# Performance work log

Measured on AMD Instinct MI355X. Metric: run time of the kernel, lower is better.

The kernel has to match this reference:

```python
import jax, jax.numpy as jnp
import numpy as np

# ----- config (matches init_kwargs) -----
DATA_SIZE = 128
WIDTH = 512
DEPTH = 3          # hidden layers in eqx.nn.MLP
NUM_BLOCKS = 2
BATCH = 512
NSTEPS = 10        # (t1 - t0) / dt0 = 1.0 / 0.1
T1 = 1.0
DT = -0.1          # integrate t1 -> t0

# Tsit5 Butcher tableau (5th-order solution weights; b7 = 0 so stage 7 is skipped)
TS_C = [0.0, 0.161, 0.327, 0.9, 0.9800255409045097, 1.0]
TS_A = [
    [],
    [0.161],
    [-0.008480655492356989, 0.335480655492357],
    [2.8971530571054935, -6.359448489975075, 4.3622954328695815],
    [5.325864828439257, -11.748883564062828, 7.4955393428898365, -0.09249506636175525],
    [5.86145544294642, -12.92096931784711, 8.159367898576159, -0.071584973281401, -0.028269050394068383],
]
TS_B = [0.09646076681806523, 0.01, 0.4798896504144996, 1.379008574103742, -3.290069515436081, 2.324710524099774]


def setup_inputs() -> dict:
    key = jax.random.key(0)
    ks = jax.random.split(key, 10)
    d, w, nb = DATA_SIZE, WIDTH, NUM_BLOCKS
    in0 = d + 1  # autonomous=False: t is concatenated to y

    def init(k, shape, fan_in):
        return jax.random.normal(k, shape, dtype=jnp.float32) / np.sqrt(fan_in).astype(np.float32)

    return {
        "y": jax.random.normal(ks[0], (BATCH, d), dtype=jnp.float32),
        "Ws0": init(ks[1], (nb, in0, w), in0), "bs0": init(ks[2], (nb, w), w),
        "Ws1": init(ks[3], (nb, w, w), w),     "bs1": init(ks[4], (nb, w), w),
        "Ws2": init(ks[5], (nb, w, w), w),     "bs2": init(ks[6], (nb, w), w),
        "Ws3": init(ks[7], (nb, w, d), w),     "bs3": init(ks[8], (nb, d), d),
    }


def _mlp(inp, layers):
    # inp: [in_size] vector (per-sample), relu hidden activations, linear output
    h = inp
    for W, b in layers[:-1]:
        h = jax.nn.relu(h @ W + b)
    W, b = layers[-1]
    return h @ W + b


def _field_and_trace(t, y, layers):
    # y: [B, d]. Exact log-det trace via vmapped vjp over identity (exact_logp_wrapper).
    eye = jnp.eye(DATA_SIZE, dtype=y.dtype)

    def single(yy):
        fn = lambda z: _mlp(jnp.concatenate([jnp.full((1,), t, yy.dtype), z]), layers)
        f, vjp_fn = jax.vjp(fn, yy)
        (dfdy,) = jax.vmap(vjp_fn)(eye)  # [d, d] Jacobian
        return f, jnp.trace(dfdy)

    return jax.vmap(single)(y)


def _solve_block(y, lp, layers):
    # Fixed-step Tsit5 on augmented state (y, logp), t1 -> t0, 10 steps.
    def step(carry, n):
        y, lp = carry
        t = jnp.float32(T1) + jnp.float32(DT) * n.astype(jnp.float32)
        ky, klp = [], []
        for i in range(6):
            ti = t + jnp.float32(TS_C[i] * DT)
            yi = y
            for j in range(i):
                yi = yi + jnp.float32(DT * TS_A[i][j]) * ky[j]
            fy, flp = _field_and_trace(ti, yi, layers)
            ky.append(fy)
            klp.append(flp)
        for i in range(6):
            y = y + jnp.float32(DT * TS_B[i]) * ky[i]
            lp = lp + jnp.float32(DT * TS_B[i]) * klp[i]
        return (y, lp), None

    (y, lp), _ = jax.lax.scan(step, (y, lp), jnp.arange(NSTEPS))
    return y, lp


def reference(y, Ws0, bs0, Ws1, bs1, Ws2, bs2, Ws3, bs3):
    lp = jnp.zeros((y.shape[0],), dtype=y.dtype)  # delta log-likelihood
    for b in range(NUM_BLOCKS):
        layers = [(Ws0[b], bs0[b]), (Ws1[b], bs1[b]), (Ws2[b], bs2[b]), (Ws3[b], bs3[b])]
        y, lp = _solve_block(y, lp, layers)
    # normal_log_likelihood (faithful to source: log(2*pi) NOT scaled by d)
    log2pi = np.float32(np.log(2.0 * np.pi))
    return lp + (-0.5) * (log2pi + jnp.sum(y * y, axis=-1))
```

## Files before the change

### kernel.cpp

```cpp
#include <hip/hip_runtime.h>


using short8 = __attribute__((ext_vector_type(8))) short;
using u16x8  = __attribute__((ext_vector_type(8))) unsigned short;
using f32x4v = __attribute__((ext_vector_type(4))) float;
using i32x4  = __attribute__((ext_vector_type(4))) int;
using u32x4  = __attribute__((ext_vector_type(4))) unsigned;

__device__ __forceinline__ unsigned short f2bf(float f) {
  union { float f; unsigned u; } v; v.f = f;
  unsigned r = v.u + 0x7fffu + ((v.u >> 16) & 1u);
  return (unsigned short)(r >> 16);
}
__device__ __forceinline__ float bf2f(unsigned short h) {
  union { unsigned u; float f; } v; v.u = ((unsigned)h) << 16; return v.f;
}
__device__ __forceinline__ signed char q8(float v, float inv) {
  float r = rintf(v * inv);
  r = fminf(fmaxf(r, -127.f), 127.f);
  return (signed char)(int)r;
}

typedef const __attribute__((address_space(1))) void gas_t;
typedef __attribute__((address_space(3))) void las_t;
__device__ __forceinline__ void gl_lds16(const void* g, void* l) {
  __builtin_amdgcn_global_load_lds((gas_t*)g, (las_t*)l, 16, 0, 0);
}

struct Coef5 { float v[5]; };
struct Coef6 { float v[6]; };

#define INV_S0 254.0f
#define INV_S1 508.0f
#define SCALE_J 7.7500155e-06f
#define SCALE_G 3.8750077e-06f

__global__ __launch_bounds__(256) void init_state(const float* __restrict__ y_in,
                                                  float* __restrict__ y,
                                                  float* __restrict__ lp) {
  int i = blockIdx.x * 256 + threadIdx.x;
  if (i < 512 * 128) y[i] = y_in[i];
  if (i < 512) lp[i] = 0.f;
}

__global__ __launch_bounds__(256) void cast_weights(
    const float* __restrict__ W0, const float* __restrict__ W1,
    const float* __restrict__ W2, const float* __restrict__ W3,
    signed char* __restrict__ w0q,
    unsigned short* __restrict__ w0tH, unsigned short* __restrict__ w0tL,
    unsigned short* __restrict__ w1tH, unsigned short* __restrict__ w1tL,
    signed char* __restrict__ w1q,
    unsigned short* __restrict__ w2tH, unsigned short* __restrict__ w2tL,
    unsigned short* __restrict__ w3tH, unsigned short* __restrict__ w3tL,
    signed char* __restrict__ w3q, signed char* __restrict__ w2q) {
  int i = blockIdx.x * 256 + threadIdx.x;
  if (i < 65536) {
    int j = i >> 9, a = i & 511;
    w0q[i] = q8(W0[(1 + j) * 512 + a], INV_S0);
    return;
  }
  i -= 65536;
  if (i >= 2 * 65536 + 2 * 262144) {
    int q = i - (2 * 65536 + 2 * 262144);
    if (q < 262144) w2q[q] = q8(W2[q], INV_S1);
    return;
  }
  float v;
  unsigned short* dh;
  unsigned short* dl;
  signed char* qd = nullptr;
  int di;
  if (i < 65536) {
    int n = i >> 7, k = i & 127;
    v = W0[(1 + k) * 512 + n]; dh = w0tH; dl = w0tL; di = i;
  } else if (i < 65536 + 262144) {
    int q = i - 65536; int n = q >> 9, k = q & 511;
    v = W1[k * 512 + n]; dh = w1tH; dl = w1tL; di = q; qd = w1q;
  } else if (i < 65536 + 2 * 262144) {
    int q = i - 65536 - 262144; int c = q >> 9, b = q & 511;
    v = W2[b * 512 + c]; dh = w2tH; dl = w2tL; di = q;
  } else {
    int q = i - 65536 - 2 * 262144; int j = q >> 9, c = q & 511;
    v = W3[c * 128 + j]; dh = w3tH; dl = w3tL; di = q; qd = w3q;
  }
  unsigned short hi = f2bf(v);
  dh[di] = hi;
  dl[di] = f2bf(v - bf2f(hi));
  if (qd) qd[di] = q8(v, INV_S1);
}

__global__ __launch_bounds__(256, 2) void fwd_l0(
    const float* __restrict__ yb, const float* __restrict__ kyb, Coef5 ca, int nc,
    const unsigned short* __restrict__ WtH, const unsigned short* __restrict__ WtL,
    const float* __restrict__ bias, const float* __restrict__ wrow0, float tval,
    unsigned short* __restrict__ Hhi, unsigned short* __restrict__ Hlo) {
  __shared__ unsigned short AsH[4096], AsL[4096], BsH[4096], BsL[4096];
  const int t = threadIdx.x, l = t & 63;
  const int wv = t >> 6, wm = wv >> 1, wn = wv & 1;
  const int lr = l & 15, lg = l >> 4, lr7 = lr & 7;
  const int m0 = blockIdx.y * 32, n0 = blockIdx.x * 32;

#pragma unroll
  for (int r = 0; r < 2; ++r) {
    int g = r * 256 + t;
    int row = g >> 4;
    int gc = (g & 15) ^ (row & 7);
    size_t bo = (size_t)(n0 + row) * 128 + gc * 8;
    int db = (r * 256 + (t & 192)) * 16;
    gl_lds16(WtH + bo, (char*)BsH + db);
    gl_lds16(WtL + bo, (char*)BsL + db);
  }
  {
    int row = t >> 3, seg = t & 7;
    int gidx = (m0 + row) * 128 + seg * 16;
    float x[16];
#pragma unroll
    for (int q = 0; q < 4; ++q) *(float4*)&x[q * 4] = *(const float4*)&yb[gidx + q * 4];
    for (int j2 = 0; j2 < nc; ++j2) {
      float c = ca.v[j2];
#pragma unroll
      for (int q = 0; q < 4; ++q) {
        float4 u = *(const float4*)&kyb[j2 * 65536 + gidx + q * 4];
        x[q * 4 + 0] = fmaf(c, u.x, x[q * 4 + 0]);
        x[q * 4 + 1] = fmaf(c, u.y, x[q * 4 + 1]);
        x[q * 4 + 2] = fmaf(c, u.z, x[q * 4 + 2]);
        x[q * 4 + 3] = fmaf(c, u.w, x[q * 4 + 3]);
      }
    }
    u16x8 h8[2], l8[2];
#pragma unroll
    for (int e = 0; e < 16; ++e) {
      unsigned short hh = f2bf(x[e]);
      h8[e >> 3][e & 7] = hh;
      l8[e >> 3][e & 7] = f2bf(x[e] - bf2f(hh));
    }
#pragma unroll
    for (int h = 0; h < 2; ++h) {
      int gx = (seg * 2 + h) ^ (row & 7);
      *(u16x8*)((char*)AsH + row * 256 + gx * 16) = h8[h];
      *(u16x8*)((char*)AsL + row * 256 + gx * 16) = l8[h];
    }
  }
  __syncthreads();

  f32x4v acc = {0.f, 0.f, 0.f, 0.f};
#pragma unroll
  for (int ks = 0; ks < 4; ++ks) {
    int sl = ((ks * 4 + lg) ^ lr7) << 4;
    int ab = (wm * 16 + lr) * 256 + sl;
    int bb = (wn * 16 + lr) * 256 + sl;
    short8 ah = *(const short8*)((const char*)AsH + ab);
    short8 al = *(const short8*)((const char*)AsL + ab);
    short8 bh = *(const short8*)((const char*)BsH + bb);
    short8 bl = *(const short8*)((const char*)BsL + bb);
    acc = __builtin_amdgcn_mfma_f32_16x16x32_bf16(ah, bh, acc, 0, 0, 0);
    acc = __builtin_amdgcn_mfma_f32_16x16x32_bf16(ah, bl, acc, 0, 0, 0);
    acc = __builtin_amdgcn_mfma_f32_16x16x32_bf16(al, bh, acc, 0, 0, 0);
  }

  int n = n0 + wn * 16 + lr;
  float be = fmaf(tval, wrow0[n], bias[n]);
#pragma unroll
  for (int r = 0; r < 4; ++r) {
    int m = m0 + wm * 16 + lg * 4 + r;
    float v = fmaxf(acc[r] + be, 0.f);
    unsigned short h = f2bf(v);
    Hhi[m * 512 + n] = h;
    Hlo[m * 512 + n] = f2bf(v - bf2f(h));
  }
}

template <bool RELU>
__global__ __launch_bounds__(256, 2) void fwd_mfma(
    const unsigned short* __restrict__ Ahi, const unsigned short* __restrict__ Alo,
    const unsigned short* __restrict__ WtH, const unsigned short* __restrict__ WtL,
    const float* __restrict__ bias,
    float* __restrict__ Cf, unsigned short* __restrict__ Hhi,
    unsigned short* __restrict__ Hlo, int N, int K) {
  __shared__ unsigned short AsH[2][4096], AsL[2][4096], BsH[2][4096], BsL[2][4096];
  const int t = threadIdx.x, l = t & 63, w = t >> 6;
  const int wm = w >> 1, wn = w & 1, lr = l & 15, lg = l >> 4;
  const int m0 = blockIdx.y * 32, n0 = blockIdx.x * 32;
  const int lr7 = lr & 7;

  auto stage = [&](int cur, int k0) {
#pragma unroll
    for (int r = 0; r < 2; ++r) {
      int g = r * 256 + t;
      int row = g >> 4, gc = g & 15;
      size_t co = (size_t)k0 + ((gc ^ (row & 7)) << 3);
      size_t ao = (size_t)(m0 + row) * K + co;
      size_t bo = (size_t)(n0 + row) * K + co;
      int db = (r * 256 + (t & 192)) * 16;
      gl_lds16(Ahi + ao, (char*)AsH[cur] + db);
      gl_lds16(Alo + ao, (char*)AsL[cur] + db);
      gl_lds16(WtH + bo, (char*)BsH[cur] + db);
      gl_lds16(WtL + bo, (char*)BsL[cur] + db);
    }
  };

  f32x4v acc = {0.f, 0.f, 0.f, 0.f};
  stage(0, 0);
  __syncthreads();
  int cur = 0;
  for (int k0 = 0; k0 < K; k0 += 128) {
    if (k0 + 128 < K) stage(cur ^ 1, k0 + 128);
#pragma unroll
    for (int ks = 0; ks < 4; ++ks) {
      int sl = ((ks * 4 + lg) ^ lr7) << 4;
      int ab = (wm * 16 + lr) * 256 + sl;
      int bb = (wn * 16 + lr) * 256 + sl;
      short8 ah = *(const short8*)((const char*)AsH[cur] + ab);
      short8 al = *(const short8*)((const char*)AsL[cur] + ab);
      short8 bh = *(const short8*)((const char*)BsH[cur] + bb);
      short8 bl = *(const short8*)((const char*)BsL[cur] + bb);
      acc = __builtin_amdgcn_mfma_f32_16x16x32_bf16(ah, bh, acc, 0, 0, 0);
      acc = __builtin_amdgcn_mfma_f32_16x16x32_bf16(ah, bl, acc, 0, 0, 0);
      acc = __builtin_amdgcn_mfma_f32_16x16x32_bf16(al, bh, acc, 0, 0, 0);
    }
    __syncthreads();
    cur ^= 1;
  }

  int n = n0 + wn * 16 + lr;
  float be = bias[n];
#pragma unroll
  for (int r = 0; r < 4; ++r) {
    int m = m0 + wm * 16 + lg * 4 + r;
    float v = acc[r] + be;
    if (RELU) {
      v = fmaxf(v, 0.f);
      unsigned short h = f2bf(v);
      Hhi[m * N + n] = h;
      Hlo[m * N + n] = f2bf(v - bf2f(h));
    } else {
      Cf[m * N + n] = v;
    }
  }
}

__global__ __launch_bounds__(256, 2) void jac_fused(
    const signed char* __restrict__ w1q, const signed char* __restrict__ w0q,
    const signed char* __restrict__ w2q, const signed char* __restrict__ w3q,
    const unsigned short* __restrict__ d0m, const unsigned short* __restrict__ d1m,
    const unsigned short* __restrict__ d2m, float* __restrict__ klp) {
  __shared__ signed char As[2][8192];
  __shared__ signed char Bs[2][8192];
  __shared__ unsigned char Ms8[3 * 2 * 512];
  __shared__ float red[8];
  const int cb = blockIdx.x, s0 = blockIdx.y * 2;
  const int t = threadIdx.x, l = t & 63, w = t >> 6;
  const int wm = w >> 1, wn = w & 1, lr = l & 15, lg = l >> 4;

  if (w < 3) {
    const unsigned short* src = (w == 0) ? d0m : (w == 1) ? d1m : d2m;
    gl_lds16(src + (size_t)s0 * 512 + l * 8, (void*)&As[0][w * 2048]);
    gl_lds16(src + (size_t)(s0 + 1) * 512 + l * 8, (void*)&As[0][w * 2048 + 1024]);
  }
  __syncthreads();
  {
    const unsigned* Mraw = (const unsigned*)&As[0][0];
    unsigned* Mout = (unsigned*)&Ms8[0];
#pragma unroll
    for (int q = 0; q < 3; ++q) {
      int i = q * 256 + t;
      unsigned lo = Mraw[2 * i], hi = Mraw[2 * i + 1];
      unsigned m = 0;
      if (lo & 0xFFFFu) m |= 0x000000FFu;
      if (lo >> 16)     m |= 0x0000FF00u;
      if (hi & 0xFFFFu) m |= 0x00FF0000u;
      if (hi >> 16)     m |= 0xFF000000u;
      Mout[i] = m;
    }
  }
  __syncthreads();

  auto stage = [&](int buf, const signed char* Aq, const signed char* Bq, int k0) {
#pragma unroll
    for (int i = 0; i < 4; ++i) {
      int u = i * 4 + w;
      if (u < 8) {
        int row = u * 16 + (l >> 2);
        gl_lds16(Aq + (size_t)(cb * 128 + row) * 512 + k0 + (l & 3) * 16,
                 (void*)&As[buf][u * 1024]);
      } else {
        int v2 = u - 8;
        int row = v2 * 16 + (l >> 2);
        gl_lds16(Bq + (size_t)row * 512 + k0 + (l & 3) * 16,
                 (void*)&Bs[buf][v2 * 1024]);
      }
    }
  };

  i32x4 a0[4][4], a1[4][4];
  auto phase = [&](const signed char* Aq, const signed char* Bq, int mbase) {
#pragma unroll
    for (int mt = 0; mt < 4; ++mt)
#pragma unroll
      for (int nt = 0; nt < 4; ++nt) {
        a0[mt][nt] = i32x4{0, 0, 0, 0};
        a1[mt][nt] = i32x4{0, 0, 0, 0};
      }
    stage(0, Aq, Bq, 0);
    __syncthreads();
    int cur = 0;
    for (int k0 = 0; k0 < 512; k0 += 64) {
      if (k0 + 64 < 512) stage(cur ^ 1, Aq, Bq, k0 + 64);
      i32x4 af[4];
#pragma unroll
      for (int mt = 0; mt < 4; ++mt)
        af[mt] = *(const i32x4*)&As[cur][(wm * 64 + mt * 16 + lr) * 64 + lg * 16];
      u32x4 mk0 = *(const u32x4*)&Ms8[mbase + k0 + lg * 16];
      u32x4 mk1 = *(const u32x4*)&Ms8[mbase + 512 + k0 + lg * 16];
#pragma unroll
      for (int nt = 0; nt < 4; ++nt) {
        u32x4 bv = *(const u32x4*)&Bs[cur][(wn * 64 + nt * 16 + lr) * 64 + lg * 16];
        i32x4 b0 = (i32x4)(bv & mk0);
        i32x4 b1 = (i32x4)(bv & mk1);
#pragma unroll
        for (int mt = 0; mt < 4; ++mt) {
          a0[mt][nt] = __builtin_amdgcn_mfma_i32_16x16x64_i8(af[mt], b0,
                                                             a0[mt][nt], 0, 0, 0);
          a1[mt][nt] = __builtin_amdgcn_mfma_i32_16x16x64_i8(af[mt], b1,
                                                             a1[mt][nt], 0, 0, 0);
        }
      }
      __syncthreads();
      cur ^= 1;
    }
  };

  phase(w2q, w3q, 2 * 1024);
  unsigned pg0[4][4][2], pg1[4][4][2];
#pragma unroll
  for (int mt = 0; mt < 4; ++mt)
#pragma unroll
    for (int nt = 0; nt < 4; ++nt) {
      float g00 = (float)a0[mt][nt][0] * SCALE_G, g01 = (float)a0[mt][nt][1] * SCALE_G;
      float g02 = (float)a0[mt][nt][2] * SCALE_G, g03 = (float)a0[mt][nt][3] * SCALE_G;
      float g10 = (float)a1[mt][nt][0] * SCALE_G, g11 = (float)a1[mt][nt][1] * SCALE_G;
      float g12 = (float)a1[mt][nt][2] * SCALE_G, g13 = (float)a1[mt][nt][3] * SCALE_G;
      asm("v_cvt_pk_bf16_f32 %0, %1, %2" : "=v"(pg0[mt][nt][0]) : "v"(g00), "v"(g01));
      asm("v_cvt_pk_bf16_f32 %0, %1, %2" : "=v"(pg0[mt][nt][1]) : "v"(g02), "v"(g03));
      asm("v_cvt_pk_bf16_f32 %0, %1, %2" : "=v"(pg1[mt][nt][0]) : "v"(g10), "v"(g11));
      asm("v_cvt_pk_bf16_f32 %0, %1, %2" : "=v"(pg1[mt][nt][1]) : "v"(g12), "v"(g13));
    }

  phase(w1q, w0q, 0);

  float p0 = 0.f, p1 = 0.f;
  const unsigned char* D1b = &Ms8[1 * 1024];
#pragma unroll
  for (int mt = 0; mt < 4; ++mt) {
    int bl = wm * 64 + mt * 16 + lg * 4;
    int blg = cb * 128 + bl;
    uchar4 m40 = *(const uchar4*)&D1b[blg];
    uchar4 m41 = *(const uchar4*)&D1b[512 + blg];
    unsigned char mm0[4] = {m40.x, m40.y, m40.z, m40.w};
    unsigned char mm1[4] = {m41.x, m41.y, m41.z, m41.w};
#pragma unroll
    for (int r = 0; r < 4; ++r) {
#pragma unroll
      for (int nt = 0; nt < 4; ++nt) {
        unsigned pw0 = pg0[mt][nt][r >> 1];
        unsigned pw1 = pg1[mt][nt][r >> 1];
        unsigned short g0 = (r & 1) ? (unsigned short)(pw0 >> 16)
                                    : (unsigned short)(pw0 & 0xFFFFu);
        unsigned short g1 = (r & 1) ? (unsigned short)(pw1 >> 16)
                                    : (unsigned short)(pw1 & 0xFFFFu);
        if (mm0[r]) p0 = fmaf((float)a0[mt][nt][r], bf2f(g0), p0);
        if (mm1[r]) p1 = fmaf((float)a1[mt][nt][r], bf2f(g1), p1);
      }
    }
  }
  p0 *= SCALE_J;
  p1 *= SCALE_J;
#pragma unroll
  for (int off = 1; off < 64; off <<= 1) {
    p0 += __shfl_xor(p0, off);
    p1 += __shfl_xor(p1, off);
  }
  if (l == 0) { red[w * 2] = p0; red[w * 2 + 1] = p1; }
  __syncthreads();
  if (t < 2) {
    klp[cb * 512 + s0 + t] = red[t] + red[2 + t] + red[4 + t] + red[6 + t];
  }
}

__global__ __launch_bounds__(256) void step_update(float* __restrict__ y,
                                                   float* __restrict__ lp,
                                                   const float* __restrict__ ky,
                                                   const float* __restrict__ klp_part,
                                                   Coef6 db) {
  int i = blockIdx.x * 256 + threadIdx.x;
  if (i < 65536) {
    float a = y[i];
#pragma unroll
    for (int j = 0; j < 6; ++j) a += db.v[j] * ky[j * 65536 + i];
    y[i] = a;
  }
  if (i < 512) {
    float l = lp[i];
#pragma unroll
    for (int j = 0; j < 6; ++j) {
      const float* kp = klp_part + j * 2048;
      float tr = kp[i] + kp[512 + i] + kp[1024 + i] + kp[1536 + i];
      l += db.v[j] * tr;
    }
    lp[i] = l;
  }
}

__global__ __launch_bounds__(64) void finalize(const float* __restrict__ y,
                                               const float* __restrict__ lp,
                                               float* __restrict__ out) {
  int s = blockIdx.x, l = threadIdx.x;
  float v0 = y[s * 128 + l], v1 = y[s * 128 + 64 + l];
  float sum = v0 * v0 + v1 * v1;
#pragma unroll
  for (int off = 32; off; off >>= 1) sum += __shfl_down(sum, off);
  if (l == 0) out[s] = lp[s] + (-0.5f) * (1.8378770664093453f + sum);
}

extern "C" void kernel_launch(void* const* d_in, const int* in_sizes, int n_in,
                              void* d_out, int out_size, void* d_ws, size_t ws_size,
                              hipStream_t stream) {
  const float* y_in = (const float*)d_in[0];
  const float* Ws0 = (const float*)d_in[1];
  const float* bs0 = (const float*)d_in[2];
  const float* Ws1 = (const float*)d_in[3];
  const float* bs1 = (const float*)d_in[4];
  const float* Ws2 = (const float*)d_in[5];
  const float* bs2 = (const float*)d_in[6];
  const float* Ws3 = (const float*)d_in[7];
  const float* bs3 = (const float*)d_in[8];
  float* out = (float*)d_out;

  char* ws = (char*)d_ws;
  size_t off = 0;
  auto alloc = [&](size_t bytes) {
    void* p = ws + off;
    off = (off + bytes + 255) & ~(size_t)255;
    return p;
  };
  float* y  = (float*)alloc(65536 * 4);
  float* lp = (float*)alloc(512 * 4);
  unsigned short* h0hi = (unsigned short*)alloc(262144 * 2);
  unsigned short* h0lo = (unsigned short*)alloc(262144 * 2);
  unsigned short* h1hi = (unsigned short*)alloc(262144 * 2);
  unsigned short* h1lo = (unsigned short*)alloc(262144 * 2);
  unsigned short* h2hi = (unsigned short*)alloc(262144 * 2);
  unsigned short* h2lo = (unsigned short*)alloc(262144 * 2);
  float* ky  = (float*)alloc(6 * 65536 * 4);
  float* klp = (float*)alloc(6 * 2048 * 4);
  unsigned short* w0tH = (unsigned short*)alloc(65536 * 2);
  unsigned short* w0tL = (unsigned short*)alloc(65536 * 2);
  unsigned short* w1tH = (unsigned short*)alloc(262144 * 2);
  unsigned short* w1tL = (unsigned short*)alloc(262144 * 2);
  unsigned short* w2tH = (unsigned short*)alloc(262144 * 2);
  unsigned short* w2tL = (unsigned short*)alloc(262144 * 2);
  unsigned short* w3tH = (unsigned short*)alloc(65536 * 2);
  unsigned short* w3tL = (unsigned short*)alloc(65536 * 2);
  signed char* w0q = (signed char*)alloc(65536);
  signed char* w1q = (signed char*)alloc(262144);
  signed char* w2q = (signed char*)alloc(262144);
  signed char* w3q = (signed char*)alloc(65536);
  (void)ws_size; (void)in_sizes; (void)n_in; (void)out_size;

  static const double DT = -0.1;
  static const double TC[6] = {0.0, 0.161, 0.327, 0.9, 0.9800255409045097, 1.0};
  static const double TA[6][5] = {
      {0, 0, 0, 0, 0},
      {0.161, 0, 0, 0, 0},
      {-0.008480655492356989, 0.335480655492357, 0, 0, 0},
      {2.8971530571054935, -6.359448489975075, 4.3622954328695815, 0, 0},
      {5.325864828439257, -11.748883564062828, 7.4955393428898365, -0.09249506636175525, 0},
      {5.86145544294642, -12.92096931784711, 8.159367898576159, -0.071584973281401,
       -0.028269050394068383}};
  static const double TB[6] = {0.09646076681806523, 0.01, 0.4798896504144996,
                               1.379008574103742, -3.290069515436081, 2.324710524099774};

  init_state<<<dim3(256), dim3(256), 0, stream>>>(y_in, y, lp);

  for (int blk = 0; blk < 2; ++blk) {
    const float* W0 = Ws0 + blk * 129 * 512;
    const float* b0 = bs0 + blk * 512;
    const float* W1 = Ws1 + blk * 262144;
    const float* b1 = bs1 + blk * 512;
    const float* W2 = Ws2 + blk * 262144;
    const float* b2 = bs2 + blk * 512;
    const float* W3 = Ws3 + blk * 65536;
    const float* b3 = bs3 + blk * 128;

    cast_weights<<<dim3(3840), dim3(256), 0, stream>>>(
        W0, W1, W2, W3, w0q, w0tH, w0tL, w1tH, w1tL, w1q,
        w2tH, w2tL, w3tH, w3tL, w3q, w2q);

    for (int n = 0; n < 10; ++n) {
      float t = 1.0f + (-0.1f) * (float)n;
      for (int i = 0; i < 6; ++i) {
        float ti = t + (float)(TC[i] * DT);
        Coef5 ca;
        for (int j = 0; j < 5; ++j) ca.v[j] = (j < i) ? (float)(DT * TA[i][j]) : 0.f;

        fwd_l0<<<dim3(16, 16), 256, 0, stream>>>(
            y, ky, ca, i, w0tH, w0tL, b0, W0, ti, h0hi, h0lo);
        fwd_mfma<true><<<dim3(16, 16), 256, 0, stream>>>(
            h0hi, h0lo, w1tH, w1tL, b1, nullptr, h1hi, h1lo, 512, 512);
        fwd_mfma<true><<<dim3(16, 16), 256, 0, stream>>>(
            h1hi, h1lo, w2tH, w2tL, b2, nullptr, h2hi, h2lo, 512, 512);
        fwd_mfma<false><<<dim3(4, 16), 256, 0, stream>>>(
            h2hi, h2lo, w3tH, w3tL, b3, ky + i * 65536, nullptr, nullptr, 128, 512);
        jac_fused<<<dim3(4, 256), 256, 0, stream>>>(
            w1q, w0q, w2q, w3q, h0hi, h1hi, h2hi, klp + i * 2048);
      }
      Coef6 db;
      for (int i2 = 0; i2 < 6; ++i2) db.v[i2] = (float)(DT * TB[i2]);
      step_update<<<dim3(256), dim3(256), 0, stream>>>(y, lp, ky, klp, db);
    }
  }
  finalize<<<dim3(512), dim3(64), 0, stream>>>(y, lp, out);
}
```

Measured before the change: 8.315 ms.

## Switch Jacobian-trace GEMMs from 16x16x64 to 32x32x32 int8 MFMA tiles

Replaces the 4x4 grid of 16x16x64 int8 MFMA tiles per wave with a 2x2 grid of 32x32x32 tiles. The LDS staging layout is reorganised into k-slices of 32 bytes so each lane reads one 16-byte fragment per tile, and the epilogue and trace reduction are remapped to the 32x32 accumulator layout. The goal is fewer MFMA issues and fewer LDS fragment loads per k-step, with better operand reuse. In exchange, the new staging pattern may change global-load coalescing and LDS bank conflicts.

```diff
diff --git a/kernel.cpp b/kernel.cpp
--- a/kernel.cpp
+++ b/kernel.cpp
@@ -6,6 +6,7 @@
 using f32x4v = __attribute__((ext_vector_type(4))) float;
 using i32x4  = __attribute__((ext_vector_type(4))) int;
 using u32x4  = __attribute__((ext_vector_type(4))) unsigned;
+using i32x16 = __attribute__((ext_vector_type(16))) int;
 
 __device__ __forceinline__ unsigned short f2bf(float f) {
   union { float f; unsigned u; } v; v.f = f;
@@ -250,7 +251,8 @@
   __shared__ float red[8];
   const int cb = blockIdx.x, s0 = blockIdx.y * 2;
   const int t = threadIdx.x, l = t & 63, w = t >> 6;
-  const int wm = w >> 1, wn = w & 1, lr = l & 15, lg = l >> 4;
+  const int wm = w >> 1, wn = w & 1;
+  const int lr31 = l & 31, hi = l >> 5;
 
   if (w < 3) {
     const unsigned short* src = (w == 0) ? d0m : (w == 1) ? d1m : d2m;
@@ -264,12 +266,12 @@
 #pragma unroll
     for (int q = 0; q < 3; ++q) {
       int i = q * 256 + t;
-      unsigned lo = Mraw[2 * i], hi = Mraw[2 * i + 1];
+      unsigned lo = Mraw[2 * i], hi2 = Mraw[2 * i + 1];
       unsigned m = 0;
       if (lo & 0xFFFFu) m |= 0x000000FFu;
       if (lo >> 16)     m |= 0x0000FF00u;
-      if (hi & 0xFFFFu) m |= 0x00FF0000u;
-      if (hi >> 16)     m |= 0xFF000000u;
+      if (hi2 & 0xFFFFu) m |= 0x00FF0000u;
+      if (hi2 >> 16)     m |= 0xFF000000u;
       Mout[i] = m;
     }
   }
@@ -279,50 +281,57 @@
 #pragma unroll
     for (int i = 0; i < 4; ++i) {
       int u = i * 4 + w;
+      int uu = (u < 8) ? u : (u - 8);
+      int g = uu * 64 + l;
+      int row = g & 127;
+      int kh = (g >> 7) & 1;
+      int ks = g >> 8;
+      int kb = k0 + ks * 32 + kh * 16;
       if (u < 8) {
-        int row = u * 16 + (l >> 2);
-        gl_lds16(Aq + (size_t)(cb * 128 + row) * 512 + k0 + (l & 3) * 16,
-                 (void*)&As[buf][u * 1024]);
+        gl_lds16(Aq + (size_t)(cb * 128 + row) * 512 + kb,
+                 (void*)&As[buf][uu * 1024]);
       } else {
-        int v2 = u - 8;
-        int row = v2 * 16 + (l >> 2);
-        gl_lds16(Bq + (size_t)row * 512 + k0 + (l & 3) * 16,
-                 (void*)&Bs[buf][v2 * 1024]);
+        gl_lds16(Bq + (size_t)row * 512 + kb, (void*)&Bs[buf][uu * 1024]);
       }
     }
   };
 
-  i32x4 a0[4][4], a1[4][4];
+  i32x16 a0[2][2], a1[2][2];
   auto phase = [&](const signed char* Aq, const signed char* Bq, int mbase) {
 #pragma unroll
-    for (int mt = 0; mt < 4; ++mt)
-#pragma unroll
-      for (int nt = 0; nt < 4; ++nt) {
-        a0[mt][nt] = i32x4{0, 0, 0, 0};
-        a1[mt][nt] = i32x4{0, 0, 0, 0};
+    for (int mt = 0; mt < 2; ++mt)
+#pragma unroll
+      for (int nt = 0; nt < 2; ++nt) {
+        a0[mt][nt] = (i32x16)(0);
+        a1[mt][nt] = (i32x16)(0);
       }
     stage(0, Aq, Bq, 0);
     __syncthreads();
     int cur = 0;
     for (int k0 = 0; k0 < 512; k0 += 64) {
       if (k0 + 64 < 512) stage(cur ^ 1, Aq, Bq, k0 + 64);
-      i32x4 af[4];
-#pragma unroll
-      for (int mt = 0; mt < 4; ++mt)
-        af[mt] = *(const i32x4*)&As[cur][(wm * 64 + mt * 16 + lr) * 64 + lg * 16];
-      u32x4 mk0 = *(const u32x4*)&Ms8[mbase + k0 + lg * 16];
-      u32x4 mk1 = *(const u32x4*)&Ms8[mbase + 512 + k0 + lg * 16];
-#pragma unroll
-      for (int nt = 0; nt < 4; ++nt) {
-        u32x4 bv = *(const u32x4*)&Bs[cur][(wn * 64 + nt * 16 + lr) * 64 + lg * 16];
-        i32x4 b0 = (i32x4)(bv & mk0);
-        i32x4 b1 = (i32x4)(bv & mk1);
-#pragma unroll
-        for (int mt = 0; mt < 4; ++mt) {
-          a0[mt][nt] = __builtin_amdgcn_mfma_i32_16x16x64_i8(af[mt], b0,
-                                                             a0[mt][nt], 0, 0, 0);
-          a1[mt][nt] = __builtin_amdgcn_mfma_i32_16x16x64_i8(af[mt], b1,
-                                                             a1[mt][nt], 0, 0, 0);
+#pragma unroll
+      for (int ks = 0; ks < 2; ++ks) {
+        i32x4 af[2];
+#pragma unroll
+        for (int mt = 0; mt < 2; ++mt)
+          af[mt] = *(const i32x4*)&As[cur][(ks * 256 + hi * 128 +
+                                            wm * 64 + mt * 32 + lr31) * 16];
+        u32x4 mk0 = *(const u32x4*)&Ms8[mbase + k0 + ks * 32 + hi * 16];
+        u32x4 mk1 = *(const u32x4*)&Ms8[mbase + 512 + k0 + ks * 32 + hi * 16];
+#pragma unroll
+        for (int nt = 0; nt < 2; ++nt) {
+          u32x4 bv = *(const u32x4*)&Bs[cur][(ks * 256 + hi * 128 +
+                                              wn * 64 + nt * 32 + lr31) * 16];
+          i32x4 b0 = (i32x4)(bv & mk0);
+          i32x4 b1 = (i32x4)(bv & mk1);
+#pragma unroll
+          for (int mt = 0; mt < 2; ++mt) {
+            a0[mt][nt] = __builtin_amdgcn_mfma_i32_32x32x32_i8(af[mt], b0,
+                                                               a0[mt][nt], 0, 0, 0);
+            a1[mt][nt] = __builtin_amdgcn_mfma_i32_32x32x32_i8(af[mt], b1,
+                                                               a1[mt][nt], 0, 0, 0);
+          }
         }
       }
       __syncthreads();
@@ -331,45 +340,48 @@
   };
 
   phase(w2q, w3q, 2 * 1024);
-  unsigned pg0[4][4][2], pg1[4][4][2];
-#pragma unroll
-  for (int mt = 0; mt < 4; ++mt)
-#pragma unroll
-    for (int nt = 0; nt < 4; ++nt) {
-      float g00 = (float)a0[mt][nt][0] * SCALE_G, g01 = (float)a0[mt][nt][1] * SCALE_G;
-      float g02 = (float)a0[mt][nt][2] * SCALE_G, g03 = (float)a0[mt][nt][3] * SCALE_G;
-      float g10 = (float)a1[mt][nt][0] * SCALE_G, g11 = (float)a1[mt][nt][1] * SCALE_G;
-      float g12 = (float)a1[mt][nt][2] * SCALE_G, g13 = (float)a1[mt][nt][3] * SCALE_G;
-      asm("v_cvt_pk_bf16_f32 %0, %1, %2" : "=v"(pg0[mt][nt][0]) : "v"(g00), "v"(g01));
-      asm("v_cvt_pk_bf16_f32 %0, %1, %2" : "=v"(pg0[mt][nt][1]) : "v"(g02), "v"(g03));
-      asm("v_cvt_pk_bf16_f32 %0, %1, %2" : "=v"(pg1[mt][nt][0]) : "v"(g10), "v"(g11));
-      asm("v_cvt_pk_bf16_f32 %0, %1, %2" : "=v"(pg1[mt][nt][1]) : "v"(g12), "v"(g13));
-    }
+  unsigned pg0[2][2][8], pg1[2][2][8];
+#pragma unroll
+  for (int mt = 0; mt < 2; ++mt)
+#pragma unroll
+    for (int nt = 0; nt < 2; ++nt)
+#pragma unroll
+      for (int p = 0; p < 8; ++p) {
+        float ga = (float)a0[mt][nt][2 * p] * SCALE_G;
+        float gb = (float)a0[mt][nt][2 * p + 1] * SCALE_G;
+        float gc = (float)a1[mt][nt][2 * p] * SCALE_G;
+        float gd = (float)a1[mt][nt][2 * p + 1] * SCALE_G;
+        asm("v_cvt_pk_bf16_f32 %0, %1, %2" : "=v"(pg0[mt][nt][p]) : "v"(ga), "v"(gb));
+        asm("v_cvt_pk_bf16_f32 %0, %1, %2" : "=v"(pg1[mt][nt][p]) : "v"(gc), "v"(gd));
+      }
 
   phase(w1q, w0q, 0);
 
   float p0 = 0.f, p1 = 0.f;
   const unsigned char* D1b = &Ms8[1 * 1024];
 #pragma unroll
-  for (int mt = 0; mt < 4; ++mt) {
-    int bl = wm * 64 + mt * 16 + lg * 4;
-    int blg = cb * 128 + bl;
-    uchar4 m40 = *(const uchar4*)&D1b[blg];
-    uchar4 m41 = *(const uchar4*)&D1b[512 + blg];
-    unsigned char mm0[4] = {m40.x, m40.y, m40.z, m40.w};
-    unsigned char mm1[4] = {m41.x, m41.y, m41.z, m41.w};
-#pragma unroll
-    for (int r = 0; r < 4; ++r) {
-#pragma unroll
-      for (int nt = 0; nt < 4; ++nt) {
-        unsigned pw0 = pg0[mt][nt][r >> 1];
-        unsigned pw1 = pg1[mt][nt][r >> 1];
-        unsigned short g0 = (r & 1) ? (unsigned short)(pw0 >> 16)
-                                    : (unsigned short)(pw0 & 0xFFFFu);
-        unsigned short g1 = (r & 1) ? (unsigned short)(pw1 >> 16)
-                                    : (unsigned short)(pw1 & 0xFFFFu);
-        if (mm0[r]) p0 = fmaf((float)a0[mt][nt][r], bf2f(g0), p0);
-        if (mm1[r]) p1 = fmaf((float)a1[mt][nt][r], bf2f(g1), p1);
+  for (int mt = 0; mt < 2; ++mt) {
+#pragma unroll
+    for (int q = 0; q < 4; ++q) {
+      int blg = cb * 128 + wm * 64 + mt * 32 + q * 8 + 4 * hi;
+      uchar4 m40 = *(const uchar4*)&D1b[blg];
+      uchar4 m41 = *(const uchar4*)&D1b[512 + blg];
+      unsigned char mm0[4] = {m40.x, m40.y, m40.z, m40.w};
+      unsigned char mm1[4] = {m41.x, m41.y, m41.z, m41.w};
+#pragma unroll
+      for (int e = 0; e < 4; ++e) {
+        const int r = q * 4 + e;
+#pragma unroll
+        for (int nt = 0; nt < 2; ++nt) {
+          unsigned pw0 = pg0[mt][nt][r >> 1];
+          unsigned pw1 = pg1[mt][nt][r >> 1];
+          unsigned short g0 = (r & 1) ? (unsigned short)(pw0 >> 16)
+                                      : (unsigned short)(pw0 & 0xFFFFu);
+          unsigned short g1 = (r & 1) ? (unsigned short)(pw1 >> 16)
+                                      : (unsigned short)(pw1 & 0xFFFFu);
+          if (mm0[e]) p0 = fmaf((float)a0[mt][nt][r], bf2f(g0), p0);
+          if (mm1[e]) p1 = fmaf((float)a1[mt][nt][r], bf2f(g1), p1);
+        }
       }
     }
   }
```

Measured after the change: 7.882 ms. 1.05x faster.
